# Performance work log

Measured on AMD Instinct MI355X. Metric: run time of the kernel, lower is better.

The kernel has to match this reference:

```python
import jax, jax.numpy as jnp
import numpy as np

# Lorenz-63 parameters (classic system this Lyapunov-spectrum code is used with)
SIGMA, RHO, BETA_P = 10.0, 28.0, 8.0 / 3.0
DT = 0.01        # time_delta
D = 3            # len_var
B = 262144       # size_tensor: ensemble of trajectories
T = 100          # len(time_sequ)


def lorenz_rhs(x, t):
    # x: [D, B]; autonomous system, t unused but kept for signature fidelity
    X, Y, Z = x[0], x[1], x[2]
    return jnp.stack([SIGMA * (Y - X), X * (RHO - Z) - Y, X * Y - BETA_P * Z])


def tangent_map(x, dt):
    # Jfunc: I + dt * Df(x), returned as [D, D, B] (row-major [row, col] layout,
    # matching multi_table/gs_table indexing of the flat list in the torch code)
    X, Y, Z = x[0], x[1], x[2]
    o = jnp.zeros_like(X)
    one = jnp.ones_like(X)
    Df = jnp.stack([
        jnp.stack([-SIGMA * one, SIGMA * one, o]),
        jnp.stack([RHO - Z, -one, -X]),
        jnp.stack([Y, X, -BETA_P * one]),
    ])  # [D, D, B]
    I = jnp.eye(D, dtype=x.dtype)[:, :, None]
    return I + dt * Df


def ode4(x, t, dt):
    k1 = lorenz_rhs(x, t)
    k2 = lorenz_rhs(x + dt * 0.5 * k1, t + dt * 0.5)
    k3 = lorenz_rhs(x + dt * 0.5 * k2, t + dt * 0.5)
    # FAITHFUL to source: k4 stage uses k2 (not k3) for the state increment
    k4 = lorenz_rhs(x + dt * k2, t + dt)
    return x + dt * (k1 + 2.0 * k2 + 2.0 * k3 + k4) * (1.0 / 6.0)


def gram_schmidt(x):
    # Classical Gram-Schmidt over COLUMNS of x [D, D, B]:
    # projections of the ORIGINAL column k onto already-orthogonalized columns i<k
    # (exactly what the torch gram_schmidt does; no normalization here)
    cols = []
    for k in range(D):
        b = x[:, k]                       # [D, B]
        for i in range(k):
            bi = cols[i]
            inner_beta = jnp.sum(bi * bi, axis=0)        # <beta_i, beta_i>  [B]
            inner_ab = jnp.sum(bi * x[:, k], axis=0)     # <beta_i, x_k>     [B]
            b = b - (inner_ab / inner_beta) * bi
        cols.append(b)
    return jnp.stack(cols, axis=1)        # [D, D, B]


def step(carry, t):
    x, Q, lya = carry
    x = ode4(x, t, DT)
    J = tangent_map(x, DT)                       # Jacobian(input_x)
    Q = jnp.einsum('ikb,kjb->ijb', J, Q)         # mat_times(Jaco, eye)
    Q = gram_schmidt(Q)
    norms = jnp.sqrt(jnp.sum(jnp.abs(Q * Q), axis=0))   # per-column norms [D, B]
    Q = Q / norms[None]                          # normalization
    lya = (lya * t + jnp.log(norms)) / (t + DT)  # running Lyapunov-exponent avg
    return (x, Q, lya), None


def setup_inputs() -> dict:
    key = jax.random.key(0)
    # initial conditions scattered around the Lorenz attractor
    x0 = jax.random.normal(key, (D, B), dtype=jnp.float32) * 0.5 \
         + jnp.array([1.0, 1.0, 20.0], dtype=jnp.float32)[:, None]
    time_sequ = jnp.arange(T, dtype=jnp.float32) * DT
    return {"x0": x0, "time_sequ": time_sequ}


def reference(x0, time_sequ):
    Bn = x0.shape[1]
    Q0 = jnp.broadcast_to(jnp.eye(D, dtype=x0.dtype)[:, :, None], (D, D, Bn))
    lya0 = jnp.zeros_like(x0)                    # [D, B]
    (x, Q, lya), _ = jax.lax.scan(step, (x0, Q0, lya0), time_sequ)
    return lya, x                                # (Lya_Spec, input_x)
```

## Files before the change

### kernel.cpp

```cpp
#include <hip/hip_runtime.h>
#include <math.h>


#define SIGMA 10.0f
#define RHO   28.0f
#define DT    0.01f
#define BETA  (8.0f / 3.0f)
#define LN2_HALF 0.34657359027997264f

typedef float f4 __attribute__((ext_vector_type(4)));

__device__ __forceinline__ f4 rcp4(f4 a) {
    f4 r;
    r.x = __builtin_amdgcn_rcpf(a.x);
    r.y = __builtin_amdgcn_rcpf(a.y);
    r.z = __builtin_amdgcn_rcpf(a.z);
    r.w = __builtin_amdgcn_rcpf(a.w);
    return r;
}
__device__ __forceinline__ f4 log2_4(f4 a) {
    f4 r;
    r.x = __builtin_amdgcn_logf(a.x);
    r.y = __builtin_amdgcn_logf(a.y);
    r.z = __builtin_amdgcn_logf(a.z);
    r.w = __builtin_amdgcn_logf(a.w);
    return r;
}

__device__ __forceinline__ void lorenz_f(f4 X, f4 Y, f4 Z, f4& fx, f4& fy, f4& fz) {
    fx = SIGMA * (Y - X);
    fy = X * (RHO - Z) - Y;
    fz = X * Y - BETA * Z;
}

__global__ __launch_bounds__(256, 1)
void lorenz_lya_kernel(const float* __restrict__ x0,
                       const float* __restrict__ ts,
                       float* __restrict__ out,
                       int B, int T) {
    int p = blockIdx.x * blockDim.x + threadIdx.x;
    int Bq = B >> 2;
    if (p >= Bq) return;

    const f4* x0v = (const f4*)x0;
    f4* outv = (f4*)out;

    f4 X = x0v[0 * Bq + p];
    f4 Y = x0v[1 * Bq + p];
    f4 Z = x0v[2 * Bq + p];

    f4 q00 = 1.0f, q01 = 0.0f, q02 = 0.0f;
    f4 q10 = 0.0f, q11 = 1.0f, q12 = 0.0f;
    f4 q20 = 0.0f, q21 = 0.0f, q22 = 1.0f;

    float t_last = ts[T - 1];

    for (int it = 0; it < T; ++it) {
        f4 k1x, k1y, k1z, k2x, k2y, k2z, k3x, k3y, k3z, k4x, k4y, k4z;
        lorenz_f(X, Y, Z, k1x, k1y, k1z);
        lorenz_f(X + (DT * 0.5f) * k1x, Y + (DT * 0.5f) * k1y, Z + (DT * 0.5f) * k1z,
                 k2x, k2y, k2z);
        lorenz_f(X + (DT * 0.5f) * k2x, Y + (DT * 0.5f) * k2y, Z + (DT * 0.5f) * k2z,
                 k3x, k3y, k3z);
        lorenz_f(X + DT * k2x, Y + DT * k2y, Z + DT * k2z,
                 k4x, k4y, k4z);
        X = X + DT * (k1x + 2.0f * k2x + 2.0f * k3x + k4x) * (1.0f / 6.0f);
        Y = Y + DT * (k1y + 2.0f * k2y + 2.0f * k3y + k4y) * (1.0f / 6.0f);
        Z = Z + DT * (k1z + 2.0f * k2z + 2.0f * k3z + k4z) * (1.0f / 6.0f);

        const f4 j10 = DT * (RHO - Z);
        const f4 j12 = -DT * X;
        const f4 j20 = DT * Y;
        const f4 j21 = DT * X;
        const float j00 = 1.0f - DT * SIGMA;
        const float j01 = DT * SIGMA;
        const float j11 = 1.0f - DT;
        const float j22 = 1.0f - DT * BETA;

        f4 n00 = j00 * q00 + j01 * q10;
        f4 n01 = j00 * q01 + j01 * q11;
        f4 n02 = j00 * q02 + j01 * q12;
        f4 n10 = j10 * q00 + j11 * q10 + j12 * q20;
        f4 n11 = j10 * q01 + j11 * q11 + j12 * q21;
        f4 n12 = j10 * q02 + j11 * q12 + j12 * q22;
        f4 n20 = j20 * q00 + j21 * q10 + j22 * q20;
        f4 n21 = j20 * q01 + j21 * q11 + j22 * q21;
        f4 n22 = j20 * q02 + j21 * q12 + j22 * q22;

        f4 ib0 = n00 * n00 + n10 * n10 + n20 * n20;
        f4 rib0 = rcp4(ib0);

        f4 d01 = n00 * n01 + n10 * n11 + n20 * n21;
        f4 c1 = d01 * rib0;
        f4 b10 = n01 - c1 * n00;
        f4 b11 = n11 - c1 * n10;
        f4 b12 = n21 - c1 * n20;

        f4 d02 = n00 * n02 + n10 * n12 + n20 * n22;
        f4 c2 = d02 * rib0;
        f4 e0 = n02 - c2 * n00;
        f4 e1 = n12 - c2 * n10;
        f4 e2 = n22 - c2 * n20;
        f4 ib1 = b10 * b10 + b11 * b11 + b12 * b12;
        f4 d12 = b10 * n02 + b11 * n12 + b12 * n22;
        f4 c3 = d12 * rcp4(ib1);
        f4 b20 = e0 - c3 * b10;
        f4 b21 = e1 - c3 * b11;
        f4 b22 = e2 - c3 * b12;

        q00 = n00;  q10 = n10;  q20 = n20;
        q01 = b10;  q11 = b11;  q21 = b12;
        q02 = b20;  q12 = b21;  q22 = b22;
    }

    f4 ib0 = q00 * q00 + q10 * q10 + q20 * q20;
    f4 ib1 = q01 * q01 + q11 * q11 + q21 * q21;
    f4 ib2 = q02 * q02 + q12 * q12 + q22 * q22;

    float scale = LN2_HALF * __builtin_amdgcn_rcpf(t_last + DT);
    outv[0 * Bq + p] = log2_4(ib0) * scale;
    outv[1 * Bq + p] = log2_4(ib1) * scale;
    outv[2 * Bq + p] = log2_4(ib2) * scale;
    outv[3 * Bq + p] = X;
    outv[4 * Bq + p] = Y;
    outv[5 * Bq + p] = Z;
}

extern "C" void kernel_launch(void* const* d_in, const int* in_sizes, int n_in,
                              void* d_out, int out_size, void* d_ws, size_t ws_size,
                              hipStream_t stream) {
    const float* x0 = (const float*)d_in[0];
    const float* ts = (const float*)d_in[1];
    float* out = (float*)d_out;
    int B = in_sizes[0] / 3;
    int T = in_sizes[1];
    int threads = 256;
    int quads = B / 4;
    int blocks = (quads + threads - 1) / threads;
    lorenz_lya_kernel<<<blocks, threads, 0, stream>>>(x0, ts, out, B, T);
}
```

Before: 102.6 us.

## Defer Gram-Schmidt reorthogonalization to once every twenty tangent steps

The tangent-matrix propagation is split into its own step function, and Gram-Schmidt now runs only after every block of 20 integration steps instead of after every step. Since no normalization is applied, the final column norms equal the product of the per-step norms in exact arithmetic. Periodic re-orthogonalization therefore gives the same result while removing most of the per-step dot products and reciprocals. The risk is reduced numerical accuracy, because columns can align and grow in magnitude between re-orthogonalizations.

```diff
diff --git a/kernel.cpp b/kernel.cpp
--- a/kernel.cpp
+++ b/kernel.cpp
@@ -7,6 +7,7 @@
 #define DT    0.01f
 #define BETA  (8.0f / 3.0f)
 #define LN2_HALF 0.34657359027997264f
+#define GS_K 20
 
 typedef float f4 __attribute__((ext_vector_type(4)));
 
@@ -33,6 +34,71 @@
     fz = X * Y - BETA * Z;
 }
 
+struct State {
+    f4 X, Y, Z;
+    f4 q00, q01, q02, q10, q11, q12, q20, q21, q22;
+};
+
+__device__ __forceinline__ void rk4_jq_step(State& s) {
+    f4 k1x, k1y, k1z, k2x, k2y, k2z, k3x, k3y, k3z, k4x, k4y, k4z;
+    lorenz_f(s.X, s.Y, s.Z, k1x, k1y, k1z);
+    lorenz_f(s.X + (DT * 0.5f) * k1x, s.Y + (DT * 0.5f) * k1y, s.Z + (DT * 0.5f) * k1z,
+             k2x, k2y, k2z);
+    lorenz_f(s.X + (DT * 0.5f) * k2x, s.Y + (DT * 0.5f) * k2y, s.Z + (DT * 0.5f) * k2z,
+             k3x, k3y, k3z);
+    lorenz_f(s.X + DT * k2x, s.Y + DT * k2y, s.Z + DT * k2z,
+             k4x, k4y, k4z);
+    s.X = s.X + DT * (k1x + 2.0f * k2x + 2.0f * k3x + k4x) * (1.0f / 6.0f);
+    s.Y = s.Y + DT * (k1y + 2.0f * k2y + 2.0f * k3y + k4y) * (1.0f / 6.0f);
+    s.Z = s.Z + DT * (k1z + 2.0f * k2z + 2.0f * k3z + k4z) * (1.0f / 6.0f);
+
+    const f4 j10 = DT * (RHO - s.Z);
+    const f4 j12 = -DT * s.X;
+    const f4 j20 = DT * s.Y;
+    const f4 j21 = DT * s.X;
+    const float j00 = 1.0f - DT * SIGMA;
+    const float j01 = DT * SIGMA;
+    const float j11 = 1.0f - DT;
+    const float j22 = 1.0f - DT * BETA;
+
+    f4 n00 = j00 * s.q00 + j01 * s.q10;
+    f4 n01 = j00 * s.q01 + j01 * s.q11;
+    f4 n02 = j00 * s.q02 + j01 * s.q12;
+    f4 n10 = j10 * s.q00 + j11 * s.q10 + j12 * s.q20;
+    f4 n11 = j10 * s.q01 + j11 * s.q11 + j12 * s.q21;
+    f4 n12 = j10 * s.q02 + j11 * s.q12 + j12 * s.q22;
+    f4 n20 = j20 * s.q00 + j21 * s.q10 + j22 * s.q20;
+    f4 n21 = j20 * s.q01 + j21 * s.q11 + j22 * s.q21;
+    f4 n22 = j20 * s.q02 + j21 * s.q12 + j22 * s.q22;
+    s.q00 = n00; s.q01 = n01; s.q02 = n02;
+    s.q10 = n10; s.q11 = n11; s.q12 = n12;
+    s.q20 = n20; s.q21 = n21; s.q22 = n22;
+}
+
+__device__ __forceinline__ void gram_schmidt(State& s) {
+    f4 ib0 = s.q00 * s.q00 + s.q10 * s.q10 + s.q20 * s.q20;
+    f4 rib0 = rcp4(ib0);
+
+    f4 d01 = s.q00 * s.q01 + s.q10 * s.q11 + s.q20 * s.q21;
+    f4 c1 = d01 * rib0;
+    f4 b10 = s.q01 - c1 * s.q00;
+    f4 b11 = s.q11 - c1 * s.q10;
+    f4 b12 = s.q21 - c1 * s.q20;
+
+    f4 d02 = s.q00 * s.q02 + s.q10 * s.q12 + s.q20 * s.q22;
+    f4 c2 = d02 * rib0;
+    f4 e0 = s.q02 - c2 * s.q00;
+    f4 e1 = s.q12 - c2 * s.q10;
+    f4 e2 = s.q22 - c2 * s.q20;
+    f4 ib1 = b10 * b10 + b11 * b11 + b12 * b12;
+    f4 d12 = b10 * s.q02 + b11 * s.q12 + b12 * s.q22;
+    f4 c3 = d12 * rcp4(ib1);
+    s.q02 = e0 - c3 * b10;
+    s.q12 = e1 - c3 * b11;
+    s.q22 = e2 - c3 * b12;
+    s.q01 = b10; s.q11 = b11; s.q21 = b12;
+}
+
 __global__ __launch_bounds__(256, 1)
 void lorenz_lya_kernel(const float* __restrict__ x0,
                        const float* __restrict__ ts,
@@ -45,85 +111,41 @@
     const f4* x0v = (const f4*)x0;
     f4* outv = (f4*)out;
 
-    f4 X = x0v[0 * Bq + p];
-    f4 Y = x0v[1 * Bq + p];
-    f4 Z = x0v[2 * Bq + p];
-
-    f4 q00 = 1.0f, q01 = 0.0f, q02 = 0.0f;
-    f4 q10 = 0.0f, q11 = 1.0f, q12 = 0.0f;
-    f4 q20 = 0.0f, q21 = 0.0f, q22 = 1.0f;
+    State s;
+    s.X = x0v[0 * Bq + p];
+    s.Y = x0v[1 * Bq + p];
+    s.Z = x0v[2 * Bq + p];
+    s.q00 = 1.0f; s.q01 = 0.0f; s.q02 = 0.0f;
+    s.q10 = 0.0f; s.q11 = 1.0f; s.q12 = 0.0f;
+    s.q20 = 0.0f; s.q21 = 0.0f; s.q22 = 1.0f;
 
     float t_last = ts[T - 1];
 
-    for (int it = 0; it < T; ++it) {
-        f4 k1x, k1y, k1z, k2x, k2y, k2z, k3x, k3y, k3z, k4x, k4y, k4z;
-        lorenz_f(X, Y, Z, k1x, k1y, k1z);
-        lorenz_f(X + (DT * 0.5f) * k1x, Y + (DT * 0.5f) * k1y, Z + (DT * 0.5f) * k1z,
-                 k2x, k2y, k2z);
-        lorenz_f(X + (DT * 0.5f) * k2x, Y + (DT * 0.5f) * k2y, Z + (DT * 0.5f) * k2z,
-                 k3x, k3y, k3z);
-        lorenz_f(X + DT * k2x, Y + DT * k2y, Z + DT * k2z,
-                 k4x, k4y, k4z);
-        X = X + DT * (k1x + 2.0f * k2x + 2.0f * k3x + k4x) * (1.0f / 6.0f);
-        Y = Y + DT * (k1y + 2.0f * k2y + 2.0f * k3y + k4y) * (1.0f / 6.0f);
-        Z = Z + DT * (k1z + 2.0f * k2z + 2.0f * k3z + k4z) * (1.0f / 6.0f);
-
-        const f4 j10 = DT * (RHO - Z);
-        const f4 j12 = -DT * X;
-        const f4 j20 = DT * Y;
-        const f4 j21 = DT * X;
-        const float j00 = 1.0f - DT * SIGMA;
-        const float j01 = DT * SIGMA;
-        const float j11 = 1.0f - DT;
-        const float j22 = 1.0f - DT * BETA;
-
-        f4 n00 = j00 * q00 + j01 * q10;
-        f4 n01 = j00 * q01 + j01 * q11;
-        f4 n02 = j00 * q02 + j01 * q12;
-        f4 n10 = j10 * q00 + j11 * q10 + j12 * q20;
-        f4 n11 = j10 * q01 + j11 * q11 + j12 * q21;
-        f4 n12 = j10 * q02 + j11 * q12 + j12 * q22;
-        f4 n20 = j20 * q00 + j21 * q10 + j22 * q20;
-        f4 n21 = j20 * q01 + j21 * q11 + j22 * q21;
-        f4 n22 = j20 * q02 + j21 * q12 + j22 * q22;
-
-        f4 ib0 = n00 * n00 + n10 * n10 + n20 * n20;
-        f4 rib0 = rcp4(ib0);
-
-        f4 d01 = n00 * n01 + n10 * n11 + n20 * n21;
-        f4 c1 = d01 * rib0;
-        f4 b10 = n01 - c1 * n00;
-        f4 b11 = n11 - c1 * n10;
-        f4 b12 = n21 - c1 * n20;
-
-        f4 d02 = n00 * n02 + n10 * n12 + n20 * n22;
-        f4 c2 = d02 * rib0;
-        f4 e0 = n02 - c2 * n00;
-        f4 e1 = n12 - c2 * n10;
-        f4 e2 = n22 - c2 * n20;
-        f4 ib1 = b10 * b10 + b11 * b11 + b12 * b12;
-        f4 d12 = b10 * n02 + b11 * n12 + b12 * n22;
-        f4 c3 = d12 * rcp4(ib1);
-        f4 b20 = e0 - c3 * b10;
-        f4 b21 = e1 - c3 * b11;
-        f4 b22 = e2 - c3 * b12;
-
-        q00 = n00;  q10 = n10;  q20 = n20;
-        q01 = b10;  q11 = b11;  q21 = b12;
-        q02 = b20;  q12 = b21;  q22 = b22;
+    int it = 0;
+    while (it < T) {
+        int kend = T - it;
+        if (kend >= GS_K) {
+            #pragma unroll 5
+            for (int u = 0; u < GS_K; ++u) rk4_jq_step(s);
+            it += GS_K;
+        } else {
+            for (int u = 0; u < kend; ++u) rk4_jq_step(s);
+            it += kend;
+        }
+        gram_schmidt(s);
     }
 
-    f4 ib0 = q00 * q00 + q10 * q10 + q20 * q20;
-    f4 ib1 = q01 * q01 + q11 * q11 + q21 * q21;
-    f4 ib2 = q02 * q02 + q12 * q12 + q22 * q22;
+    f4 ib0 = s.q00 * s.q00 + s.q10 * s.q10 + s.q20 * s.q20;
+    f4 ib1 = s.q01 * s.q01 + s.q11 * s.q11 + s.q21 * s.q21;
+    f4 ib2 = s.q02 * s.q02 + s.q12 * s.q12 + s.q22 * s.q22;
 
     float scale = LN2_HALF * __builtin_amdgcn_rcpf(t_last + DT);
     outv[0 * Bq + p] = log2_4(ib0) * scale;
     outv[1 * Bq + p] = log2_4(ib1) * scale;
     outv[2 * Bq + p] = log2_4(ib2) * scale;
-    outv[3 * Bq + p] = X;
-    outv[4 * Bq + p] = Y;
-    outv[5 * Bq + p] = Z;
+    outv[3 * Bq + p] = s.X;
+    outv[4 * Bq + p] = s.Y;
+    outv[5 * Bq + p] = s.Z;
 }
 
 extern "C" void kernel_launch(void* const* d_in, const int* in_sizes, int n_in,
```

Result: faster. 88.06 us (-14.2%).
